# Kernel tuning notes

Hardware: AMD Instinct MI355X
Metric: run time of the kernel (lower is better)

## Reference

```python
import jax, jax.numpy as jnp
import numpy as np

H, W = 100, 100  # local_env_shape


def setup_inputs() -> dict:
    key = jax.random.key(0)
    k1, = jax.random.split(key, 1)
    B, T, P = 32, 10, 25
    # points in [0, 110): with resolution=1, origin=0 most land in the 100x100 grid,
    x = jax.random.uniform(k1, (B, T, 2 * P), dtype=jnp.float32) * 110.0
    resolution = jnp.ones((B, T, 2), dtype=jnp.float32)
    origin = jnp.zeros((B, T, 2), dtype=jnp.float32)
    return {"x": x, "resolution": resolution, "origin": origin}


def reference(x, resolution, origin):
    B, T, n = x.shape
    P = n // 2
    points = x.reshape(B, T, P, 2)  # [B, T, P, 2] (x, y)
    # row index from y-coordinate, col index from x-coordinate (cast truncates, as tf.cast does)
    row = (points[..., 1] / resolution[:, :, 0:1] + origin[:, :, 0:1]).astype(jnp.int32)  # [B,T,P]
    col = (points[..., 0] / resolution[:, :, 1:2] + origin[:, :, 1:2]).astype(jnp.int32)  # [B,T,P]
    in_bounds = (row >= 0) & (row < H) & (col >= 0) & (col < W)  # [B,T,P]
    row_safe = jnp.clip(row, 0, H - 1)
    col_safe = jnp.clip(col, 0, W - 1)
    b_idx = jnp.arange(B)[:, None, None]
    t_idx = jnp.arange(T)[None, :, None]
    p_idx = jnp.arange(P)[None, None, :]
    grid = jnp.zeros((B, T, H, W, P), dtype=jnp.float32)
    # scatter-max so masked-out (OOB) points write 0 and never clobber a valid 1
    out = grid.at[b_idx, t_idx, row_safe, col_safe, p_idx].max(in_bounds.astype(jnp.float32))
    return out
```

## Files before the change

kernel.cpp:

```cpp
#include <hip/hip_runtime.h>

#define BB 32
#define TT 10
#define PP 25
#define HH 100
#define WW 100

__global__ void raster_scatter_kernel(const float* __restrict__ x,
                                      const float* __restrict__ resolution,
                                      const float* __restrict__ origin,
                                      float* __restrict__ out) {
    int tid = blockIdx.x * blockDim.x + threadIdx.x;
    const int N = BB * TT * PP;
    if (tid >= N) return;

    int p  = tid % PP;
    int bt = tid / PP;

    const float px = x[bt * (2 * PP) + 2 * p];
    const float py = x[bt * (2 * PP) + 2 * p + 1];
    const float r0 = resolution[bt * 2 + 0];
    const float r1 = resolution[bt * 2 + 1];
    const float o0 = origin[bt * 2 + 0];
    const float o1 = origin[bt * 2 + 1];

    int row = (int)(py / r0 + o0);
    int col = (int)(px / r1 + o1);

    if (row >= 0 && row < HH && col >= 0 && col < WW) {
        size_t idx = (((size_t)bt * HH + (size_t)row) * WW + (size_t)col) * PP + (size_t)p;
        out[idx] = 1.0f;
    }
}

extern "C" void kernel_launch(void* const* d_in, const int* in_sizes, int n_in,
                              void* d_out, int out_size, void* d_ws, size_t ws_size,
                              hipStream_t stream) {
    const float* x          = (const float*)d_in[0];
    const float* resolution = (const float*)d_in[1];
    const float* origin     = (const float*)d_in[2];
    float* out = (float*)d_out;

    hipMemsetAsync(out, 0, (size_t)out_size * sizeof(float), stream);

    const int N = BB * TT * PP;
    raster_scatter_kernel<<<(N + 255) / 256, 256, 0, stream>>>(x, resolution, origin, out);
}
```

Measured before the change: 312.4 us.

## Replace memset plus scatter with a single dense vectorized fill kernel

Drops the separate memset and sparse scatter. One kernel now writes every output element with float4 stores, comparing each element's cell against point cells staged in shared memory. This removes the second pass over the output and a launch, in exchange for extra per-element index arithmetic and a shared-memory lookup.

```diff
diff --git a/kernel.cpp b/kernel.cpp
--- a/kernel.cpp
+++ b/kernel.cpp
@@ -6,31 +6,46 @@
 #define HH 100
 #define WW 100
 
-__global__ void raster_scatter_kernel(const float* __restrict__ x,
-                                      const float* __restrict__ resolution,
-                                      const float* __restrict__ origin,
-                                      float* __restrict__ out) {
-    int tid = blockIdx.x * blockDim.x + threadIdx.x;
-    const int N = BB * TT * PP;
-    if (tid >= N) return;
+__global__ __launch_bounds__(256) void raster_dense_kernel(
+        const float* __restrict__ x,
+        const float* __restrict__ resolution,
+        const float* __restrict__ origin,
+        float* __restrict__ out) {
+    const int bt  = blockIdx.y;
+    const int tid = threadIdx.x;
 
-    int p  = tid % PP;
-    int bt = tid / PP;
+    __shared__ int cell[PP];
+    if (tid < PP) {
+        const float px = x[bt * (2 * PP) + 2 * tid];
+        const float py = x[bt * (2 * PP) + 2 * tid + 1];
+        const float r0 = resolution[bt * 2 + 0];
+        const float r1 = resolution[bt * 2 + 1];
+        const float o0 = origin[bt * 2 + 0];
+        const float o1 = origin[bt * 2 + 1];
+        const int row = (int)(py / r0 + o0);
+        const int col = (int)(px / r1 + o1);
+        cell[tid] = (row >= 0 && row < HH && col >= 0 && col < WW)
+                        ? (row * WW + col) : -1;
+    }
+    __syncthreads();
 
-    const float px = x[bt * (2 * PP) + 2 * p];
-    const float py = x[bt * (2 * PP) + 2 * p + 1];
-    const float r0 = resolution[bt * 2 + 0];
-    const float r1 = resolution[bt * 2 + 1];
-    const float o0 = origin[bt * 2 + 0];
-    const float o1 = origin[bt * 2 + 1];
+    const int i4 = blockIdx.x * 256 + tid;
+    const int N4 = (HH * WW * PP) / 4;
+    if (i4 >= N4) return;
 
-    int row = (int)(py / r0 + o0);
-    int col = (int)(px / r1 + o1);
+    const int e = i4 * 4;
+    int p  = e % PP;
+    int hw = e / PP;
 
-    if (row >= 0 && row < HH && col >= 0 && col < WW) {
-        size_t idx = (((size_t)bt * HH + (size_t)row) * WW + (size_t)col) * PP + (size_t)p;
-        out[idx] = 1.0f;
+    float vals[4];
+#pragma unroll
+    for (int j = 0; j < 4; ++j) {
+        vals[j] = (cell[p] == hw) ? 1.0f : 0.0f;
+        if (++p == PP) { p = 0; ++hw; }
     }
+
+    float4 v = make_float4(vals[0], vals[1], vals[2], vals[3]);
+    *reinterpret_cast<float4*>(out + (size_t)bt * (HH * WW * PP) + e) = v;
 }
 
 extern "C" void kernel_launch(void* const* d_in, const int* in_sizes, int n_in,
@@ -41,8 +56,7 @@
     const float* origin     = (const float*)d_in[2];
     float* out = (float*)d_out;
 
-    hipMemsetAsync(out, 0, (size_t)out_size * sizeof(float), stream);
-
-    const int N = BB * TT * PP;
-    raster_scatter_kernel<<<(N + 255) / 256, 256, 0, stream>>>(x, resolution, origin, out);
+    const int N4 = (HH * WW * PP) / 4;
+    dim3 grid((N4 + 255) / 256, BB * TT);
+    raster_dense_kernel<<<grid, 256, 0, stream>>>(x, resolution, origin, out);
 }
```

After: 343.0 us. 1.1x slower.
